# Kernel tuning notes

Hardware: AMD Instinct MI355X
Metric: run time of the kernel (lower is better)

The kernel has to match this reference:

```python
import jax, jax.numpy as jnp
import numpy as np

M, N, D, P = 16, 4096, 128, 8192
H = N // D


def setup_inputs() -> dict:
    key = jax.random.key(0)
    ks = jax.random.split(key, 6)
    s = 1.0 / np.sqrt(N)
    return {
        "X": jax.random.normal(ks[0], (M, N), dtype=jnp.float32),
        "W_q": jax.random.normal(ks[1], (N, N), dtype=jnp.float32) * s,
        "W_k": jax.random.normal(ks[2], (N, N), dtype=jnp.float32) * s,
        "W_v": jax.random.normal(ks[3], (N, N), dtype=jnp.float32) * s,
        "cache_K": jax.random.normal(ks[4], (H, P, D), dtype=jnp.float32),
        "cache_V": jax.random.normal(ks[5], (H, P, D), dtype=jnp.float32),
    }


def reference(X, W_q, W_k, W_v, cache_K, cache_V):
    m = X.shape[0]
    h, p, d = cache_K.shape
    # QKV projections: [M, N] @ [N, N] -> [M, H, D] -> [H, M, D]
    q = (X @ W_q).reshape(m, h, d).transpose(1, 0, 2)
    k = (X @ W_k).reshape(m, h, d).transpose(1, 0, 2)
    v = (X @ W_v).reshape(m, h, d).transpose(1, 0, 2)
    # KV-cache concat along the sequence axis -> [H, P+M, D]
    k_all = jnp.concatenate([cache_K, k], axis=1)
    v_all = jnp.concatenate([cache_V, v], axis=1)
    # attention (note: original applies NO 1/sqrt(D) scaling)
    scores = jnp.einsum('hmd,hpd->hmp', q, k_all)  # [H, M, P+M]
    weights = jax.nn.softmax(scores, axis=-1)
    out = jnp.einsum('hmp,hpd->hmd', weights, v_all)  # [H, M, D]
    return out.transpose(1, 0, 2).reshape(m, h * d)
```

## Files before the change

### kernel.cpp

```cpp
#include <hip/hip_runtime.h>

#define HN 32
#define MM 16
#define DD 128
#define NN 4096
#define PP 8192
#define TP 64

__global__ __launch_bounds__(256) void qkv_kernel(
    const float* __restrict__ X, const float* __restrict__ Wq,
    const float* __restrict__ Wk, const float* __restrict__ Wv,
    float* __restrict__ qkv)
{
    __shared__ float Xs[MM][128];
    const int bx  = blockIdx.x;
    const int mat = bx >> 8;
    const int r   = bx & 255;
    const int ct  = r >> 5;
    const int rc  = r & 31;
    const int col0 = ct << 9;
    const int i0   = rc << 7;
    const float* W = (mat == 0) ? Wq : (mat == 1) ? Wk : Wv;
    const int t = threadIdx.x;

    for (int f = t; f < MM*128; f += 256)
        Xs[f >> 7][f & 127] = X[(f >> 7)*NN + i0 + (f & 127)];
    __syncthreads();

    const int c0 = col0 + 2*t;
    float a0[MM], a1[MM];
#pragma unroll
    for (int m = 0; m < MM; ++m) { a0[m] = 0.f; a1[m] = 0.f; }

    for (int i4 = 0; i4 < 128; i4 += 4) {
        const float* Wr = W + (size_t)(i0 + i4) * NN + c0;
        float2 w0 = *reinterpret_cast<const float2*>(Wr);
        float2 w1 = *reinterpret_cast<const float2*>(Wr + NN);
        float2 w2 = *reinterpret_cast<const float2*>(Wr + 2*NN);
        float2 w3 = *reinterpret_cast<const float2*>(Wr + 3*NN);
#pragma unroll
        for (int m = 0; m < MM; ++m) {
            float4 x = *reinterpret_cast<const float4*>(&Xs[m][i4]);
            a0[m] += x.x*w0.x + x.y*w1.x + x.z*w2.x + x.w*w3.x;
            a1[m] += x.x*w0.y + x.y*w1.y + x.z*w2.y + x.w*w3.y;
        }
    }
    const int h0 = c0 >> 7, d0 = c0 & 127;
    float* base = qkv + (size_t)mat * HN*MM*DD + (size_t)h0*MM*DD + d0;
#pragma unroll
    for (int m = 0; m < MM; ++m) {
        atomicAdd(base + m*DD,     a0[m]);
        atomicAdd(base + m*DD + 1, a1[m]);
    }
}

__global__ __launch_bounds__(256, 4) void attn_partial2(
    const float* __restrict__ cacheK, const float* __restrict__ cacheV,
    const float* __restrict__ qkv, float* __restrict__ pmu,
    float* __restrict__ ps, float* __restrict__ pacc,
    int nch, int chunklen)
{
    __shared__ float KV[TP][DD + 4];
    __shared__ float Wl[MM][68];

    const int chunk = blockIdx.x;
    const int h     = blockIdx.y;
    const int t     = threadIdx.x;
    const int lane  = t & 63;
    const int w     = __builtin_amdgcn_readfirstlane((int)(threadIdx.x >> 6));
    const int psi   = lane >> 4;
    const int g     = lane & 15;

    const float* k_ws = qkv + HN*MM*DD;
    const float* v_ws = qkv + 2*HN*MM*DD;
    const float* qb   = qkv + (size_t)(h*MM + 4*w)*DD;

    const int cnt   = (chunk < nch - 1) ? chunklen : MM;
    const int ntile = (cnt + TP - 1) / TP;

    float mu0 = -3.0e38f, mu1 = -3.0e38f, mu2 = -3.0e38f, mu3 = -3.0e38f;
    float ss0 = 0.f, ss1 = 0.f, ss2 = 0.f, ss3 = 0.f;
    float acc[4][8];
#pragma unroll
    for (int q = 0; q < 4; ++q)
#pragma unroll
        for (int k = 0; k < 8; ++k) acc[q][k] = 0.f;

    const int srow = t >> 5, sc4 = t & 31;

    for (int tt = 0; tt < ntile; ++tt) {
        const int t0 = tt * TP;
        const int valid = min(TP, cnt - t0);

        __syncthreads();
#pragma unroll
        for (int rr = 0; rr < 8; ++rr) {
            const int r2 = srow + rr*8;
            float4 v = make_float4(0.f, 0.f, 0.f, 0.f);
            if (r2 < valid) {
                const float* kp = (chunk < nch - 1)
                    ? cacheK + ((size_t)h*PP + (size_t)chunk*chunklen + t0 + r2)*DD
                    : k_ws + (size_t)(h*MM + t0 + r2)*DD;
                v = reinterpret_cast<const float4*>(kp)[sc4];
            }
            *reinterpret_cast<float4*>(&KV[r2][sc4*4]) = v;
        }
        __syncthreads();

        float s0 = 0.f, s1 = 0.f, s2 = 0.f, s3 = 0.f;
#pragma unroll 8
        for (int dq = 0; dq < 32; ++dq) {
            float4 k = *reinterpret_cast<const float4*>(&KV[lane][dq*4]);
            const float* qp = qb + dq*4;
            float4 q0 = *reinterpret_cast<const float4*>(qp);
            float4 q1 = *reinterpret_cast<const float4*>(qp + DD);
            float4 q2 = *reinterpret_cast<const float4*>(qp + 2*DD);
            float4 q3 = *reinterpret_cast<const float4*>(qp + 3*DD);
            s0 += k.x*q0.x + k.y*q0.y + k.z*q0.z + k.w*q0.w;
            s1 += k.x*q1.x + k.y*q1.y + k.z*q1.z + k.w*q1.w;
            s2 += k.x*q2.x + k.y*q2.y + k.z*q2.z + k.w*q2.w;
            s3 += k.x*q3.x + k.y*q3.y + k.z*q3.z + k.w*q3.w;
        }
        if (lane >= valid) { s0 = s1 = s2 = s3 = -3.0e38f; }
        __syncthreads();

#pragma unroll
        for (int rr = 0; rr < 8; ++rr) {
            const int r2 = srow + rr*8;
            float4 v = make_float4(0.f, 0.f, 0.f, 0.f);
            if (r2 < valid) {
                const float* vp = (chunk < nch - 1)
                    ? cacheV + ((size_t)h*PP + (size_t)chunk*chunklen + t0 + r2)*DD
                    : v_ws + (size_t)(h*MM + t0 + r2)*DD;
                v = reinterpret_cast<const float4*>(vp)[sc4];
            }
            *reinterpret_cast<float4*>(&KV[r2][sc4*4]) = v;
        }

        float m0 = s0, m1 = s1, m2 = s2, m3 = s3;
#pragma unroll
        for (int off = 1; off < 64; off <<= 1) {
            m0 = fmaxf(m0, __shfl_xor(m0, off));
            m1 = fmaxf(m1, __shfl_xor(m1, off));
            m2 = fmaxf(m2, __shfl_xor(m2, off));
            m3 = fmaxf(m3, __shfl_xor(m3, off));
        }
        const float n0 = fmaxf(mu0, m0), n1 = fmaxf(mu1, m1);
        const float n2 = fmaxf(mu2, m2), n3 = fmaxf(mu3, m3);
        const float r0 = __expf(mu0 - n0), r1 = __expf(mu1 - n1);
        const float r2_ = __expf(mu2 - n2), r3 = __expf(mu3 - n3);
        float w0 = (lane < valid) ? __expf(s0 - n0) : 0.f;
        float w1 = (lane < valid) ? __expf(s1 - n1) : 0.f;
        float w2 = (lane < valid) ? __expf(s2 - n2) : 0.f;
        float w3 = (lane < valid) ? __expf(s3 - n3) : 0.f;
        float t0s = w0, t1s = w1, t2s = w2, t3s = w3;
#pragma unroll
        for (int off = 1; off < 64; off <<= 1) {
            t0s += __shfl_xor(t0s, off);
            t1s += __shfl_xor(t1s, off);
            t2s += __shfl_xor(t2s, off);
            t3s += __shfl_xor(t3s, off);
        }
        ss0 = ss0*r0 + t0s; ss1 = ss1*r1 + t1s;
        ss2 = ss2*r2_ + t2s; ss3 = ss3*r3 + t3s;
        mu0 = n0; mu1 = n1; mu2 = n2; mu3 = n3;
        Wl[4*w + 0][lane] = w0;
        Wl[4*w + 1][lane] = w1;
        Wl[4*w + 2][lane] = w2;
        Wl[4*w + 3][lane] = w3;
        __syncthreads();

#pragma unroll
        for (int k = 0; k < 8; ++k) {
            acc[0][k] *= r0; acc[1][k] *= r1; acc[2][k] *= r2_; acc[3][k] *= r3;
        }
#pragma unroll 4
        for (int p = psi; p < TP; p += 4) {
            float wq[4];
            wq[0] = Wl[4*w + 0][p];
            wq[1] = Wl[4*w + 1][p];
            wq[2] = Wl[4*w + 2][p];
            wq[3] = Wl[4*w + 3][p];
            float4 v0 = *reinterpret_cast<const float4*>(&KV[p][g*8]);
            float4 v1 = *reinterpret_cast<const float4*>(&KV[p][g*8 + 4]);
#pragma unroll
            for (int q = 0; q < 4; ++q) {
                acc[q][0] += wq[q]*v0.x; acc[q][1] += wq[q]*v0.y;
                acc[q][2] += wq[q]*v0.z; acc[q][3] += wq[q]*v0.w;
                acc[q][4] += wq[q]*v1.x; acc[q][5] += wq[q]*v1.y;
                acc[q][6] += wq[q]*v1.z; acc[q][7] += wq[q]*v1.w;
            }
        }
    }

#pragma unroll
    for (int q = 0; q < 4; ++q)
#pragma unroll
        for (int k = 0; k < 8; ++k) {
            float v = acc[q][k];
            v += __shfl_xor(v, 16);
            v += __shfl_xor(v, 32);
            acc[q][k] = v;
        }
    if (psi == 0) {
        float* pa = pacc + ((size_t)(h*nch + chunk)*MM + 4*w)*DD;
#pragma unroll
        for (int q = 0; q < 4; ++q) {
            *reinterpret_cast<float4*>(pa + q*DD + g*8) =
                make_float4(acc[q][0], acc[q][1], acc[q][2], acc[q][3]);
            *reinterpret_cast<float4*>(pa + q*DD + g*8 + 4) =
                make_float4(acc[q][4], acc[q][5], acc[q][6], acc[q][7]);
        }
    }
    if (lane == 0) {
        const int o = (h*nch + chunk)*MM + 4*w;
        pmu[o + 0] = mu0; pmu[o + 1] = mu1; pmu[o + 2] = mu2; pmu[o + 3] = mu3;
        ps [o + 0] = ss0; ps [o + 1] = ss1; ps [o + 2] = ss2; ps [o + 3] = ss3;
    }
}

__global__ __launch_bounds__(128) void combine_kernel(
    const float* __restrict__ pmu, const float* __restrict__ ps,
    const float* __restrict__ pacc, float* __restrict__ out, int nch)
{
    const int b = blockIdx.x;
    const int h = b >> 4, m = b & 15;
    const int d = threadIdx.x;
    float gm = -3.0e38f;
    for (int c = 0; c < nch; ++c)
        gm = fmaxf(gm, pmu[(h*nch + c)*MM + m]);
    float stot = 0.f, a = 0.f;
    for (int c = 0; c < nch; ++c) {
        const float f = __expf(pmu[(h*nch + c)*MM + m] - gm);
        stot += ps[(h*nch + c)*MM + m] * f;
        a += pacc[((size_t)(h*nch + c)*MM + m)*DD + d] * f;
    }
    out[m*NN + h*DD + d] = a / stot;
}

static size_t ws_need_floats(int nch) {
    return (size_t)3*HN*MM*DD + 2*(size_t)HN*nch*MM + (size_t)HN*nch*MM*DD;
}

extern "C" void kernel_launch(void* const* d_in, const int* in_sizes, int n_in,
                              void* d_out, int out_size, void* d_ws, size_t ws_size,
                              hipStream_t stream) {
    const float* X  = (const float*)d_in[0];
    const float* Wq = (const float*)d_in[1];
    const float* Wk = (const float*)d_in[2];
    const float* Wv = (const float*)d_in[3];
    const float* cK = (const float*)d_in[4];
    const float* cV = (const float*)d_in[5];
    float* out = (float*)d_out;

    int nch = 65;
    if (ws_size < ws_need_floats(65)*sizeof(float)) nch = 33;
    if (ws_size < ws_need_floats(33)*sizeof(float)) nch = 17;
    const int chunklen = PP / (nch - 1);

    float* ws     = (float*)d_ws;
    float* qkv    = ws;
    float* pmu_p  = ws + 3*HN*MM*DD;
    float* ps_p   = pmu_p + (size_t)HN*nch*MM;
    float* pacc_p = ps_p + (size_t)HN*nch*MM;

    hipMemsetAsync(qkv, 0, (size_t)3*HN*MM*DD*sizeof(float), stream);
    qkv_kernel<<<768, 256, 0, stream>>>(X, Wq, Wk, Wv, qkv);
    attn_partial2<<<dim3(nch, HN), 256, 0, stream>>>(cK, cV, qkv, pmu_p, ps_p, pacc_p,
                                                     nch, chunklen);
    combine_kernel<<<HN*MM, 128, 0, stream>>>(pmu_p, ps_p, pacc_p, out, nch);
}
```

Baseline: 205.0 us.

## Prefetch K/V tiles through registers with separate LDS buffers, fix chunk count

The attention kernel now keeps separate shared-memory buffers for K and V. Each tile's global loads go into registers ahead of time, so the next K tile and the current V tile are fetched while the scores and softmax are computed, and one barrier per tile is dropped. The chunk count is fixed at 16, which gives 512 blocks instead of up to 2080. The softmax weight layout becomes transposed so each weight read is a single float4. The QKV kernel reads scalar columns 256 apart over 8 rows at a time instead of float2 pairs. Risks: fewer blocks and more registers (launch bounds lowered to 2) may cost occupancy and parallelism on a GPU with many CUs.

Result: faster. 174.7 us (-14.8%).

```diff
diff --git a/kernel.cpp b/kernel.cpp
--- a/kernel.cpp
+++ b/kernel.cpp
@@ -6,6 +6,8 @@
 #define NN 4096
 #define PP 8192
 #define TP 64
+#define NCH 16
+#define CHUNKLEN (PP / NCH)
 
 __global__ __launch_bounds__(256) void qkv_kernel(
     const float* __restrict__ X, const float* __restrict__ Wq,
@@ -27,56 +29,66 @@
         Xs[f >> 7][f & 127] = X[(f >> 7)*NN + i0 + (f & 127)];
     __syncthreads();
 
-    const int c0 = col0 + 2*t;
+    const int c0 = col0 + t, c1 = col0 + 256 + t;
     float a0[MM], a1[MM];
 #pragma unroll
     for (int m = 0; m < MM; ++m) { a0[m] = 0.f; a1[m] = 0.f; }
 
-    for (int i4 = 0; i4 < 128; i4 += 4) {
-        const float* Wr = W + (size_t)(i0 + i4) * NN + c0;
-        float2 w0 = *reinterpret_cast<const float2*>(Wr);
-        float2 w1 = *reinterpret_cast<const float2*>(Wr + NN);
-        float2 w2 = *reinterpret_cast<const float2*>(Wr + 2*NN);
-        float2 w3 = *reinterpret_cast<const float2*>(Wr + 3*NN);
+    for (int i8 = 0; i8 < 128; i8 += 8) {
+        const float* Wr = W + (size_t)(i0 + i8) * NN;
+        float w0[8], w1[8];
+#pragma unroll
+        for (int rr = 0; rr < 8; ++rr) {
+            w0[rr] = Wr[rr*NN + c0];
+            w1[rr] = Wr[rr*NN + c1];
+        }
 #pragma unroll
         for (int m = 0; m < MM; ++m) {
-            float4 x = *reinterpret_cast<const float4*>(&Xs[m][i4]);
-            a0[m] += x.x*w0.x + x.y*w1.x + x.z*w2.x + x.w*w3.x;
-            a1[m] += x.x*w0.y + x.y*w1.y + x.z*w2.y + x.w*w3.y;
-        }
-    }
+            float4 xa = *reinterpret_cast<const float4*>(&Xs[m][i8]);
+            float4 xb = *reinterpret_cast<const float4*>(&Xs[m][i8 + 4]);
+            a0[m] += xa.x*w0[0] + xa.y*w0[1] + xa.z*w0[2] + xa.w*w0[3]
+                   + xb.x*w0[4] + xb.y*w0[5] + xb.z*w0[6] + xb.w*w0[7];
+            a1[m] += xa.x*w1[0] + xa.y*w1[1] + xa.z*w1[2] + xa.w*w1[3]
+                   + xb.x*w1[4] + xb.y*w1[5] + xb.z*w1[6] + xb.w*w1[7];
+        }
+    }
+    float* base = qkv + (size_t)mat * HN*MM*DD;
     const int h0 = c0 >> 7, d0 = c0 & 127;
-    float* base = qkv + (size_t)mat * HN*MM*DD + (size_t)h0*MM*DD + d0;
+    const int h1 = c1 >> 7, d1 = c1 & 127;
 #pragma unroll
     for (int m = 0; m < MM; ++m) {
-        atomicAdd(base + m*DD,     a0[m]);
-        atomicAdd(base + m*DD + 1, a1[m]);
-    }
-}
-
-__global__ __launch_bounds__(256, 4) void attn_partial2(
+        atomicAdd(&base[(h0*MM + m)*DD + d0], a0[m]);
+        atomicAdd(&base[(h1*MM + m)*DD + d1], a1[m]);
+    }
+}
+
+__global__ __launch_bounds__(256, 2) void attn_partial3(
     const float* __restrict__ cacheK, const float* __restrict__ cacheV,
     const float* __restrict__ qkv, float* __restrict__ pmu,
-    float* __restrict__ ps, float* __restrict__ pacc,
-    int nch, int chunklen)
+    float* __restrict__ ps, float* __restrict__ pacc)
 {
-    __shared__ float KV[TP][DD + 4];
-    __shared__ float Wl[MM][68];
+    __shared__ float KA[TP][DD + 4];
+    __shared__ float KB[TP][DD + 4];
+    __shared__ float Wl[TP][20];
 
     const int chunk = blockIdx.x;
     const int h     = blockIdx.y;
     const int t     = threadIdx.x;
     const int lane  = t & 63;
-    const int w     = __builtin_amdgcn_readfirstlane((int)(threadIdx.x >> 6));
+    const int wv    = t >> 6;
+    const int srow0 = t >> 5;
+    const int sg    = t & 31;
     const int psi   = lane >> 4;
     const int g     = lane & 15;
 
     const float* k_ws = qkv + HN*MM*DD;
     const float* v_ws = qkv + 2*HN*MM*DD;
-    const float* qb   = qkv + (size_t)(h*MM + 4*w)*DD;
-
-    const int cnt   = (chunk < nch - 1) ? chunklen : MM;
-    const int ntile = (cnt + TP - 1) / TP;
+    const float* Kbase = cacheK + ((size_t)h*PP + (size_t)chunk*CHUNKLEN)*DD;
+    const float* Vbase = cacheV + ((size_t)h*PP + (size_t)chunk*CHUNKLEN)*DD;
+    const float* qb    = qkv + ((size_t)h*MM + 4*wv)*DD;
+
+    const int nfull = CHUNKLEN / TP;
+    const int ntile = nfull + (chunk == NCH - 1 ? 1 : 0);
 
     float mu0 = -3.0e38f, mu1 = -3.0e38f, mu2 = -3.0e38f, mu3 = -3.0e38f;
     float ss0 = 0.f, ss1 = 0.f, ss2 = 0.f, ss3 = 0.f;
@@ -86,31 +98,58 @@
 #pragma unroll
         for (int k = 0; k < 8; ++k) acc[q][k] = 0.f;
 
-    const int srow = t >> 5, sc4 = t & 31;
+    float4 stK[8], stV[8];
+
+    auto issueK = [&](int tt2) {
+        if (tt2 < nfull) {
+            const float* B = Kbase + (size_t)(tt2*TP)*DD;
+#pragma unroll
+            for (int rr = 0; rr < 8; ++rr)
+                stK[rr] = *reinterpret_cast<const float4*>(B + (size_t)(srow0 + 8*rr)*DD + sg*4);
+        } else {
+#pragma unroll
+            for (int rr = 0; rr < 8; ++rr) {
+                const int row = srow0 + 8*rr;
+                stK[rr] = (row < MM)
+                    ? *reinterpret_cast<const float4*>(k_ws + ((size_t)h*MM + row)*DD + sg*4)
+                    : make_float4(0.f, 0.f, 0.f, 0.f);
+            }
+        }
+    };
+    auto issueV = [&](int tt2) {
+        if (tt2 < nfull) {
+            const float* B = Vbase + (size_t)(tt2*TP)*DD;
+#pragma unroll
+            for (int rr = 0; rr < 8; ++rr)
+                stV[rr] = *reinterpret_cast<const float4*>(B + (size_t)(srow0 + 8*rr)*DD + sg*4);
+        } else {
+#pragma unroll
+            for (int rr = 0; rr < 8; ++rr) {
+                const int row = srow0 + 8*rr;
+                stV[rr] = (row < MM)
+                    ? *reinterpret_cast<const float4*>(v_ws + ((size_t)h*MM + row)*DD + sg*4)
+                    : make_float4(0.f, 0.f, 0.f, 0.f);
+            }
+        }
+    };
+
+    issueK(0);
 
     for (int tt = 0; tt < ntile; ++tt) {
-        const int t0 = tt * TP;
-        const int valid = min(TP, cnt - t0);
+        const int valid = (tt < nfull) ? TP : MM;
+
+#pragma unroll
+        for (int rr = 0; rr < 8; ++rr)
+            *reinterpret_cast<float4*>(&KA[srow0 + 8*rr][sg*4]) = stK[rr];
+
+        issueV(tt);
 
         __syncthreads();
-#pragma unroll
-        for (int rr = 0; rr < 8; ++rr) {
-            const int r2 = srow + rr*8;
-            float4 v = make_float4(0.f, 0.f, 0.f, 0.f);
-            if (r2 < valid) {
-                const float* kp = (chunk < nch - 1)
-                    ? cacheK + ((size_t)h*PP + (size_t)chunk*chunklen + t0 + r2)*DD
-                    : k_ws + (size_t)(h*MM + t0 + r2)*DD;
-                v = reinterpret_cast<const float4*>(kp)[sc4];
-            }
-            *reinterpret_cast<float4*>(&KV[r2][sc4*4]) = v;
-        }
-        __syncthreads();
 
         float s0 = 0.f, s1 = 0.f, s2 = 0.f, s3 = 0.f;
-#pragma unroll 8
+#pragma unroll 4
         for (int dq = 0; dq < 32; ++dq) {
-            float4 k = *reinterpret_cast<const float4*>(&KV[lane][dq*4]);
+            float4 k = *reinterpret_cast<const float4*>(&KA[lane][dq*4]);
             const float* qp = qb + dq*4;
             float4 q0 = *reinterpret_cast<const float4*>(qp);
             float4 q1 = *reinterpret_cast<const float4*>(qp + DD);
@@ -122,20 +161,12 @@
             s3 += k.x*q3.x + k.y*q3.y + k.z*q3.z + k.w*q3.w;
         }
         if (lane >= valid) { s0 = s1 = s2 = s3 = -3.0e38f; }
-        __syncthreads();
-
-#pragma unroll
-        for (int rr = 0; rr < 8; ++rr) {
-            const int r2 = srow + rr*8;
-            float4 v = make_float4(0.f, 0.f, 0.f, 0.f);
-            if (r2 < valid) {
-                const float* vp = (chunk < nch - 1)
-                    ? cacheV + ((size_t)h*PP + (size_t)chunk*chunklen + t0 + r2)*DD
-                    : v_ws + (size_t)(h*MM + t0 + r2)*DD;
-                v = reinterpret_cast<const float4*>(vp)[sc4];
-            }
-            *reinterpret_cast<float4*>(&KV[r2][sc4*4]) = v;
-        }
+
+#pragma unroll
+        for (int rr = 0; rr < 8; ++rr)
+            *reinterpret_cast<float4*>(&KB[srow0 + 8*rr][sg*4]) = stV[rr];
+
+        if (tt + 1 < ntile) issueK(tt + 1);
 
         float m0 = s0, m1 = s1, m2 = s2, m3 = s3;
 #pragma unroll
@@ -164,10 +195,8 @@
         ss0 = ss0*r0 + t0s; ss1 = ss1*r1 + t1s;
         ss2 = ss2*r2_ + t2s; ss3 = ss3*r3 + t3s;
         mu0 = n0; mu1 = n1; mu2 = n2; mu3 = n3;
-        Wl[4*w + 0][lane] = w0;
-        Wl[4*w + 1][lane] = w1;
-        Wl[4*w + 2][lane] = w2;
-        Wl[4*w + 3][lane] = w3;
+        *reinterpret_cast<float4*>(&Wl[lane][4*wv]) = make_float4(w0, w1, w2, w3);
+
         __syncthreads();
 
 #pragma unroll
@@ -175,21 +204,19 @@
             acc[0][k] *= r0; acc[1][k] *= r1; acc[2][k] *= r2_; acc[3][k] *= r3;
         }
 #pragma unroll 4
-        for (int p = psi; p < TP; p += 4) {
-            float wq[4];
-            wq[0] = Wl[4*w + 0][p];
-            wq[1] = Wl[4*w + 1][p];
-            wq[2] = Wl[4*w + 2][p];
-            wq[3] = Wl[4*w + 3][p];
-            float4 v0 = *reinterpret_cast<const float4*>(&KV[p][g*8]);
-            float4 v1 = *reinterpret_cast<const float4*>(&KV[p][g*8 + 4]);
-#pragma unroll
-            for (int q = 0; q < 4; ++q) {
-                acc[q][0] += wq[q]*v0.x; acc[q][1] += wq[q]*v0.y;
-                acc[q][2] += wq[q]*v0.z; acc[q][3] += wq[q]*v0.w;
-                acc[q][4] += wq[q]*v1.x; acc[q][5] += wq[q]*v1.y;
-                acc[q][6] += wq[q]*v1.z; acc[q][7] += wq[q]*v1.w;
-            }
+        for (int i = 0; i < 16; ++i) {
+            const int p = psi + 4*i;
+            float4 wq = *reinterpret_cast<const float4*>(&Wl[p][4*wv]);
+            float4 v0 = *reinterpret_cast<const float4*>(&KB[p][g*8]);
+            float4 v1 = *reinterpret_cast<const float4*>(&KB[p][g*8 + 4]);
+            acc[0][0] += wq.x*v0.x; acc[0][1] += wq.x*v0.y; acc[0][2] += wq.x*v0.z; acc[0][3] += wq.x*v0.w;
+            acc[0][4] += wq.x*v1.x; acc[0][5] += wq.x*v1.y; acc[0][6] += wq.x*v1.z; acc[0][7] += wq.x*v1.w;
+            acc[1][0] += wq.y*v0.x; acc[1][1] += wq.y*v0.y; acc[1][2] += wq.y*v0.z; acc[1][3] += wq.y*v0.w;
+            acc[1][4] += wq.y*v1.x; acc[1][5] += wq.y*v1.y; acc[1][6] += wq.y*v1.z; acc[1][7] += wq.y*v1.w;
+            acc[2][0] += wq.z*v0.x; acc[2][1] += wq.z*v0.y; acc[2][2] += wq.z*v0.z; acc[2][3] += wq.z*v0.w;
+            acc[2][4] += wq.z*v1.x; acc[2][5] += wq.z*v1.y; acc[2][6] += wq.z*v1.z; acc[2][7] += wq.z*v1.w;
+            acc[3][0] += wq.w*v0.x; acc[3][1] += wq.w*v0.y; acc[3][2] += wq.w*v0.z; acc[3][3] += wq.w*v0.w;
+            acc[3][4] += wq.w*v1.x; acc[3][5] += wq.w*v1.y; acc[3][6] += wq.w*v1.z; acc[3][7] += wq.w*v1.w;
         }
     }
 
@@ -203,7 +230,7 @@
             acc[q][k] = v;
         }
     if (psi == 0) {
-        float* pa = pacc + ((size_t)(h*nch + chunk)*MM + 4*w)*DD;
+        float* pa = pacc + ((size_t)(h*NCH + chunk)*MM + 4*wv)*DD;
 #pragma unroll
         for (int q = 0; q < 4; ++q) {
             *reinterpret_cast<float4*>(pa + q*DD + g*8) =
@@ -213,7 +240,7 @@
         }
     }
     if (lane == 0) {
-        const int o = (h*nch + chunk)*MM + 4*w;
+        const int o = (h*NCH + chunk)*MM + 4*wv;
         pmu[o + 0] = mu0; pmu[o + 1] = mu1; pmu[o + 2] = mu2; pmu[o + 3] = mu3;
         ps [o + 0] = ss0; ps [o + 1] = ss1; ps [o + 2] = ss2; ps [o + 3] = ss3;
     }
@@ -221,25 +248,23 @@
 
 __global__ __launch_bounds__(128) void combine_kernel(
     const float* __restrict__ pmu, const float* __restrict__ ps,
-    const float* __restrict__ pacc, float* __restrict__ out, int nch)
+    const float* __restrict__ pacc, float* __restrict__ out)
 {
     const int b = blockIdx.x;
     const int h = b >> 4, m = b & 15;
     const int d = threadIdx.x;
     float gm = -3.0e38f;
-    for (int c = 0; c < nch; ++c)
-        gm = fmaxf(gm, pmu[(h*nch + c)*MM + m]);
+#pragma unroll
+    for (int c = 0; c < NCH; ++c)
+        gm = fmaxf(gm, pmu[(h*NCH + c)*MM + m]);
     float stot = 0.f, a = 0.f;
-    for (int c = 0; c < nch; ++c) {
-        const float f = __expf(pmu[(h*nch + c)*MM + m] - gm);
-        stot += ps[(h*nch + c)*MM + m] * f;
-        a += pacc[((size_t)(h*nch + c)*MM + m)*DD + d] * f;
+#pragma unroll
+    for (int c = 0; c < NCH; ++c) {
+        const float f = __expf(pmu[(h*NCH + c)*MM + m] - gm);
+        stot += ps[(h*NCH + c)*MM + m] * f;
+        a += pacc[((size_t)(h*NCH + c)*MM + m)*DD + d] * f;
     }
     out[m*NN + h*DD + d] = a / stot;
-}
-
-static size_t ws_need_floats(int nch) {
-    return (size_t)3*HN*MM*DD + 2*(size_t)HN*nch*MM + (size_t)HN*nch*MM*DD;
 }
 
 extern "C" void kernel_launch(void* const* d_in, const int* in_sizes, int n_in,
@@ -253,20 +278,14 @@
     const float* cV = (const float*)d_in[5];
     float* out = (float*)d_out;
 
-    int nch = 65;
-    if (ws_size < ws_need_floats(65)*sizeof(float)) nch = 33;
-    if (ws_size < ws_need_floats(33)*sizeof(float)) nch = 17;
-    const int chunklen = PP / (nch - 1);
-
     float* ws     = (float*)d_ws;
     float* qkv    = ws;
     float* pmu_p  = ws + 3*HN*MM*DD;
-    float* ps_p   = pmu_p + (size_t)HN*nch*MM;
-    float* pacc_p = ps_p + (size_t)HN*nch*MM;
+    float* ps_p   = pmu_p + HN*NCH*MM;
+    float* pacc_p = ps_p + HN*NCH*MM;
 
     hipMemsetAsync(qkv, 0, (size_t)3*HN*MM*DD*sizeof(float), stream);
     qkv_kernel<<<768, 256, 0, stream>>>(X, Wq, Wk, Wv, qkv);
-    attn_partial2<<<dim3(nch, HN), 256, 0, stream>>>(cK, cV, qkv, pmu_p, ps_p, pacc_p,
-                                                     nch, chunklen);
-    combine_kernel<<<HN*MM, 128, 0, stream>>>(pmu_p, ps_p, pacc_p, out, nch);
-}
+    attn_partial3<<<dim3(NCH, HN), 256, 0, stream>>>(cK, cV, qkv, pmu_p, ps_p, pacc_p);
+    combine_kernel<<<HN*MM, 128, 0, stream>>>(pmu_p, ps_p, pacc_p, out);
+}
```
